# Kernel optimization log

Measured on AMD Instinct MI355X. Metric: run time of the kernel, lower is better.

Reference implementation:

```python
import jax, jax.numpy as jnp
import numpy as np

N_NODES = 10000
N_EDGES = 640000
D_FEAT = 128
D_OUT = 128


def setup_inputs() -> dict:
    key = jax.random.key(0)
    ks = jax.random.split(key, 7)
    feat = jax.random.normal(ks[0], (N_NODES, D_FEAT), dtype=jnp.float32)
    # src_fc: Linear(D_FEAT, D_FEAT); fc: Linear(2*D_FEAT, D_OUT). torch Linear weight is [out, in].
    W_src = jax.random.normal(ks[1], (D_FEAT, D_FEAT), dtype=jnp.float32) * (1.0 / np.sqrt(D_FEAT))
    b_src = jax.random.normal(ks[2], (D_FEAT,), dtype=jnp.float32) * 0.01
    W_fc = jax.random.normal(ks[3], (D_OUT, 2 * D_FEAT), dtype=jnp.float32) * (1.0 / np.sqrt(2 * D_FEAT))
    b_fc = jax.random.normal(ks[4], (D_OUT,), dtype=jnp.float32) * 0.01
    src = jax.random.randint(ks[5], (N_EDGES,), 0, N_NODES, dtype=jnp.int32)
    dst = jax.random.randint(ks[6], (N_EDGES,), 0, N_NODES, dtype=jnp.int32)
    return {"feat": feat, "W_src": W_src, "b_src": b_src, "W_fc": W_fc, "b_fc": b_fc,
            "src": src, "dst": dst}


def reference(feat, W_src, b_src, W_fc, b_fc, src, dst):
    """SAGEConv forward (eval mode: dropout = identity, activation = identity).

    message: m_e = src_fc(feat[src_e])                 # [E, D]
    reduce:  neigh_v = mean_{e: dst_e = v} m_e         # [N, D]
    apply:   h_v = fc(concat(feat_v, neigh_v))         # [N, D_out]
    """
    n = feat.shape[0]
    # gather src features and apply per-edge linear transform
    m = feat[src] @ W_src.T + b_src                                  # [E, D]
    # segment mean over destination nodes (nodes with no in-edges get 0,
    # matching DGL's zero-initialized dstdata)
    agg = jax.ops.segment_sum(m, dst, num_segments=n)                # [N, D]
    deg = jax.ops.segment_sum(jnp.ones(dst.shape, feat.dtype), dst, num_segments=n)
    neigh = agg / jnp.maximum(deg, 1.0)[:, None]                     # [N, D]
    h = jnp.concatenate([feat, neigh], axis=-1) @ W_fc.T + b_fc      # [N, D_out]
    return h
```

## Files before the change

kernel.cpp:

```cpp
#include <hip/hip_runtime.h>

#define NN 10000
#define DF 128
#define NE 640000
#define GBN 16
#define NBUCK 625
#define TILE 8192
#define NTILES ((NE + TILE - 1) / TILE)
#define EPT 8
#define GCAP 2048

#define PACK_BLKS 625
#define PREP_BLKS 16

typedef __attribute__((ext_vector_type(8))) short bf16x8;
typedef __attribute__((ext_vector_type(4))) float f32x4;
typedef unsigned long long ull;

__device__ __forceinline__ unsigned int f2bf(float f) {
    unsigned int u = __float_as_uint(f);
    u = (u + 0x7FFFu + ((u >> 16) & 1u)) >> 16;
    return u;
}
__device__ __forceinline__ unsigned int pack2bf(float a, float b) {
    return f2bf(a) | (f2bf(b) << 16);
}
__device__ __forceinline__ float bf_lo(unsigned int v) { return __uint_as_float(v << 16); }
__device__ __forceinline__ float bf_hi(unsigned int v) { return __uint_as_float(v & 0xFFFF0000u); }

__global__ __launch_bounds__(1024) void prologue(const float* __restrict__ feat,
                                                 unsigned int* __restrict__ A_bf,
                                                 const int* __restrict__ dstv,
                                                 int* __restrict__ tbl,
                                                 const float* __restrict__ Wfc,
                                                 const float* __restrict__ Wsrc,
                                                 const float* __restrict__ bsrc,
                                                 unsigned int* __restrict__ Bw,
                                                 float* __restrict__ bsrc2)
{
    const int bx = blockIdx.x, tid = threadIdx.x;

    if (bx < PACK_BLKS) {
        const int id = bx * 1024 + tid;
        const int row = id >> 6, j = id & 63;
        const float2 f = *(const float2*)(feat + (size_t)row * DF + 2 * j);
        A_bf[(size_t)row * 64 + j] = pack2bf(f.x, f.y);
        return;
    }
    if (bx < PACK_BLKS + NTILES) {
        __shared__ int h[NBUCK];
        const int t = bx - PACK_BLKS;
        if (tid < NBUCK) h[tid] = 0;
        __syncthreads();
        const int e0 = t * TILE;
#pragma unroll
        for (int j = 0; j < EPT; ++j) {
            const int e = e0 + j * 1024 + tid;
            if (e < NE) atomicAdd(&h[dstv[e] >> 4], 1);
        }
        __syncthreads();
        if (tid < NBUCK) tbl[t * NBUCK + tid] = h[tid];
        return;
    }
    {
        __shared__ float wp[8][128];
        __shared__ float red[16];
        const int g = tid >> 7;
        const int k = tid & 127;
        const int o = (bx - PACK_BLKS - NTILES) * 8 + g;
        const float* w2 = Wfc + (size_t)o * 256 + 128;
        float acc = 0.f;
#pragma unroll 8
        for (int j = 0; j < 128; ++j)
            acc = fmaf(w2[j], Wsrc[j * 128 + k], acc);
        wp[g][k] = acc;

        float p = w2[k] * bsrc[k];
#pragma unroll
        for (int d = 32; d > 0; d >>= 1) p += __shfl_down(p, d);
        if ((tid & 63) == 0) red[tid >> 6] = p;
        __syncthreads();
        if (k < 64) {
            const float2 wf = *(const float2*)(Wfc + (size_t)o * 256 + 2 * k);
            Bw[(size_t)o * 128 + k] = pack2bf(wf.x, wf.y);
            Bw[(size_t)o * 128 + 64 + k] = pack2bf(wp[g][2 * k], wp[g][2 * k + 1]);
        }
        if (k == 0) bsrc2[o] = red[2 * g] + red[2 * g + 1];
    }
}

__global__ __launch_bounds__(1024) void bin2(const int* __restrict__ srcv,
                                             const int* __restrict__ dstv,
                                             const int* __restrict__ tbl,
                                             unsigned int* __restrict__ ents,
                                             int* __restrict__ off_g)
{
    __shared__ unsigned int ent[TILE];
    __shared__ ull sc[1024];
    __shared__ int lbase[NBUCK];
    __shared__ int lcur[NBUCK];
    __shared__ int gbase[NBUCK];

    const int tid = threadIdx.x;
    const int bx = blockIdx.x;
    const int e0 = bx * TILE;
    const int n = min(TILE, NE - e0);

    int myd[EPT], mys[EPT];
#pragma unroll
    for (int j = 0; j < EPT; ++j) {
        const int e = e0 + j * 1024 + tid;
        if (e < NE) { myd[j] = dstv[e]; mys[j] = srcv[e]; }
        else { myd[j] = -1; mys[j] = 0; }
    }

    int pre = 0, tot = 0, myh = 0;
    if (tid < NBUCK) {
        for (int t = 0; t < NTILES; ++t) {
            const int c = tbl[t * NBUCK + tid];
            pre += (t < bx) ? c : 0;
            myh += (t == bx) ? c : 0;
            tot += c;
        }
    }
    sc[tid] = (tid < NBUCK) ? (((ull)(unsigned)tot << 32) | (unsigned)myh) : 0ull;
    __syncthreads();
    for (int d = 1; d < 1024; d <<= 1) {
        ull x = (tid >= d) ? sc[tid - d] : 0ull;
        __syncthreads();
        sc[tid] += x;
        __syncthreads();
    }
    const ull ex = (tid == 0) ? 0ull : sc[tid - 1];
    if (tid < NBUCK) {
        const int offb = (int)(ex >> 32);
        lbase[tid] = (int)(ex & 0xFFFFFFFFull);
        gbase[tid] = offb + pre;
        lcur[tid] = 0;
        if (bx == 0) off_g[tid] = offb;
    }
    if (bx == 0 && tid == NBUCK - 1) off_g[NBUCK] = (int)(sc[NBUCK - 1] >> 32);
    __syncthreads();

#pragma unroll
    for (int j = 0; j < EPT; ++j) {
        if (myd[j] >= 0) {
            const int b = myd[j] >> 4;
            const int p = atomicAdd(&lcur[b], 1);
            ent[lbase[b] + p] = ((unsigned)myd[j] << 14) | (unsigned)mys[j];
        }
    }
    __syncthreads();

    for (int i = tid; i < n; i += 1024) {
        const unsigned u = ent[i];
        const int b = (int)(u >> 18);
        ents[gbase[b] + (i - lbase[b])] = u;
    }
}

__global__ __launch_bounds__(256) void gather_apply(const unsigned int* __restrict__ A_bf,
                                                    const unsigned int* __restrict__ Bw,
                                                    const unsigned int* __restrict__ ents,
                                                    const int* __restrict__ off,
                                                    const float* __restrict__ bfc,
                                                    const float* __restrict__ bsrc2,
                                                    float* __restrict__ out)
{
    __shared__ unsigned int raw[GCAP];
    __shared__ unsigned short sorted[GCAP];
    __shared__ int h[GBN], base[GBN], cur[GBN];
    __shared__ unsigned int ntile[GBN][68];

    const int tid = threadIdx.x;
    const int b = blockIdx.x;
    const int rbase = b * GBN;
    const int r0 = off[b], r1 = off[b + 1];
    const int cnt = min(r1 - r0, GCAP);

    if (tid < GBN) { h[tid] = 0; cur[tid] = 0; }
    __syncthreads();
    for (int i = tid; i < cnt; i += 256) {
        const unsigned u = ents[r0 + i];
        raw[i] = u;
        atomicAdd(&h[(u >> 14) & (GBN - 1)], 1);
    }
    __syncthreads();
    if (tid == 0) {
        int s = 0;
#pragma unroll
        for (int j = 0; j < GBN; ++j) { base[j] = s; s += h[j]; }
    }
    __syncthreads();
    for (int i = tid; i < cnt; i += 256) {
        const unsigned u = raw[i];
        const int dl = (int)((u >> 14) & (GBN - 1));
        const int p = base[dl] + atomicAdd(&cur[dl], 1);
        sorted[p] = (unsigned short)(u & 0x3FFFu);
    }
    __syncthreads();

    const int wave = tid >> 6, lane = tid & 63;
#pragma unroll
    for (int j = 0; j < 4; ++j) {
        const int dl = wave * 4 + j;
        const int s0 = base[dl], n = h[dl];
        float ax = 0.f, ay = 0.f;
        int i = 0;
        for (; i + 4 <= n; i += 4) {
            const int ia = sorted[s0 + i + 0];
            const int ib = sorted[s0 + i + 1];
            const int ic = sorted[s0 + i + 2];
            const int id = sorted[s0 + i + 3];
            const unsigned a  = A_bf[(size_t)ia * 64 + lane];
            const unsigned bb = A_bf[(size_t)ib * 64 + lane];
            const unsigned c  = A_bf[(size_t)ic * 64 + lane];
            const unsigned d  = A_bf[(size_t)id * 64 + lane];
            ax += (bf_lo(a) + bf_lo(bb)) + (bf_lo(c) + bf_lo(d));
            ay += (bf_hi(a) + bf_hi(bb)) + (bf_hi(c) + bf_hi(d));
        }
        for (; i < n; ++i) {
            const unsigned a = A_bf[(size_t)sorted[s0 + i] * 64 + lane];
            ax += bf_lo(a); ay += bf_hi(a);
        }
        const float inv = (n > 0) ? 1.f / (float)n : 0.f;
        ntile[dl][lane] = pack2bf(ax * inv, ay * inv);
    }
    __syncthreads();

    const int wv = wave;
    const int r = lane & 15, kg = lane >> 4;

    const unsigned int* ap = A_bf + (size_t)(rbase + r) * 64 + kg * 4;
    bf16x8 a[8];
#pragma unroll
    for (int s = 0; s < 4; ++s) a[s] = *(const bf16x8*)(ap + s * 16);
#pragma unroll
    for (int s = 0; s < 4; ++s) a[4 + s] = *(const bf16x8*)(&ntile[r][s * 16 + kg * 4]);

    bool hd[4];
#pragma unroll
    for (int q = 0; q < 4; ++q) hd[q] = h[kg * 4 + q] > 0;

#pragma unroll
    for (int half = 0; half < 2; ++half) {
        const int cbase = (wv * 2 + half) * 16;
        const unsigned int* bp = Bw + (size_t)(cbase + r) * 128 + kg * 4;
        bf16x8 bb[8];
#pragma unroll
        for (int s = 0; s < 8; ++s) bb[s] = *(const bf16x8*)(bp + s * 16);
        f32x4 acc = {0.f, 0.f, 0.f, 0.f};
#pragma unroll
        for (int s = 0; s < 8; ++s)
            acc = __builtin_amdgcn_mfma_f32_16x16x32_bf16(a[s], bb[s], acc, 0, 0, 0);

        const int col = cbase + r;
        const float bc = bfc[col], bs = bsrc2[col];
#pragma unroll
        for (int q = 0; q < 4; ++q) {
            const int row = rbase + kg * 4 + q;
            out[(size_t)row * DF + col] = acc[q] + bc + (hd[q] ? bs : 0.f);
        }
    }
}

extern "C" void kernel_launch(void* const* d_in, const int* in_sizes, int n_in,
                              void* d_out, int out_size, void* d_ws, size_t ws_size,
                              hipStream_t stream) {
    const float* feat  = (const float*)d_in[0];
    const float* W_src = (const float*)d_in[1];
    const float* b_src = (const float*)d_in[2];
    const float* W_fc  = (const float*)d_in[3];
    const float* b_fc  = (const float*)d_in[4];
    const int*   src   = (const int*)d_in[5];
    const int*   dst   = (const int*)d_in[6];
    float* out = (float*)d_out;

    unsigned int* A_bf = (unsigned int*)d_ws;
    unsigned int* Bw = A_bf + (size_t)NN * 64;
    float* bsrc2 = (float*)(Bw + 128 * 128);
    int*   off   = (int*)(bsrc2 + 128);
    int*   tbl   = off + (NBUCK + 1);
    unsigned int* ents = (unsigned int*)(tbl + (size_t)NTILES * NBUCK);

    prologue    <<<PACK_BLKS + NTILES + PREP_BLKS, 1024, 0, stream>>>(
                    feat, A_bf, dst, tbl, W_fc, W_src, b_src, Bw, bsrc2);
    bin2        <<<NTILES, 1024, 0, stream>>>(src, dst, tbl, ents, off);
    gather_apply<<<NBUCK, 256, 0, stream>>>(A_bf, Bw, ents, off, b_fc, bsrc2, out);
}
```

Before: 56.46 us.

## Vectorize bf16 packing, use wave-shuffle scan, double gather_apply threads

The feature-to-bf16 pack now has each thread convert 8 floats with 128-bit loads and stores, so it needs far fewer blocks. The bucket prefix scan in bin2 replaces the 1024-entry shared-memory Hillis-Steele scan, which needed many barriers, with wave shuffles plus a small per-wave partial sum. gather_apply now runs 512 threads per block: each wave aggregates 2 destination rows with 8 loads in flight instead of 4 rows with 4, and computes one 16-column MFMA tile instead of two. The aim is more parallelism and memory-level parallelism in the latency-bound gather, at the cost of more registers per thread and higher block-size pressure.

```diff
diff --git a/kernel.cpp b/kernel.cpp
--- a/kernel.cpp
+++ b/kernel.cpp
@@ -10,7 +10,7 @@
 #define EPT 8
 #define GCAP 2048
 
-#define PACK_BLKS 625
+#define PACK_BLKS 157
 #define PREP_BLKS 16
 
 typedef __attribute__((ext_vector_type(8))) short bf16x8;
@@ -42,9 +42,15 @@
 
     if (bx < PACK_BLKS) {
         const int id = bx * 1024 + tid;
-        const int row = id >> 6, j = id & 63;
-        const float2 f = *(const float2*)(feat + (size_t)row * DF + 2 * j);
-        A_bf[(size_t)row * 64 + j] = pack2bf(f.x, f.y);
+        if (id < NN * 16) {
+            const int row = id >> 4, j4 = id & 15;
+            const float4 fa = *(const float4*)(feat + (size_t)row * DF + 8 * j4);
+            const float4 fb = *(const float4*)(feat + (size_t)row * DF + 8 * j4 + 4);
+            uint4 v;
+            v.x = pack2bf(fa.x, fa.y); v.y = pack2bf(fa.z, fa.w);
+            v.z = pack2bf(fb.x, fb.y); v.w = pack2bf(fb.z, fb.w);
+            *(uint4*)(A_bf + (size_t)row * 64 + 4 * j4) = v;
+        }
         return;
     }
     if (bx < PACK_BLKS + NTILES) {
@@ -96,12 +102,13 @@
                                              int* __restrict__ off_g)
 {
     __shared__ unsigned int ent[TILE];
-    __shared__ ull sc[1024];
+    __shared__ ull wpart[16];
     __shared__ int lbase[NBUCK];
     __shared__ int lcur[NBUCK];
     __shared__ int gbase[NBUCK];
 
     const int tid = threadIdx.x;
+    const int lane = tid & 63, wid = tid >> 6;
     const int bx = blockIdx.x;
     const int e0 = bx * TILE;
     const int n = min(TILE, NE - e0);
@@ -123,23 +130,28 @@
             tot += c;
         }
     }
-    sc[tid] = (tid < NBUCK) ? (((ull)(unsigned)tot << 32) | (unsigned)myh) : 0ull;
-    __syncthreads();
-    for (int d = 1; d < 1024; d <<= 1) {
-        ull x = (tid >= d) ? sc[tid - d] : 0ull;
-        __syncthreads();
-        sc[tid] += x;
-        __syncthreads();
-    }
-    const ull ex = (tid == 0) ? 0ull : sc[tid - 1];
+    const ull v = (tid < NBUCK) ? (((ull)(unsigned)tot << 32) | (unsigned)myh) : 0ull;
+    ull inc = v;
+#pragma unroll
+    for (int d = 1; d < 64; d <<= 1) {
+        const ull x = (ull)__shfl_up((unsigned long long)inc, d);
+        if (lane >= d) inc += x;
+    }
+    if (lane == 63) wpart[wid] = inc;
+    __syncthreads();
+    ull wsum = 0;
+    for (int w = 0; w < wid; ++w) wsum += wpart[w];
+    const ull ex = wsum + inc - v;
     if (tid < NBUCK) {
         const int offb = (int)(ex >> 32);
         lbase[tid] = (int)(ex & 0xFFFFFFFFull);
         gbase[tid] = offb + pre;
         lcur[tid] = 0;
-        if (bx == 0) off_g[tid] = offb;
-    }
-    if (bx == 0 && tid == NBUCK - 1) off_g[NBUCK] = (int)(sc[NBUCK - 1] >> 32);
+        if (bx == 0) {
+            off_g[tid] = offb;
+            if (tid == NBUCK - 1) off_g[NBUCK] = (int)((ex + v) >> 32);
+        }
+    }
     __syncthreads();
 
 #pragma unroll
@@ -159,7 +171,7 @@
     }
 }
 
-__global__ __launch_bounds__(256) void gather_apply(const unsigned int* __restrict__ A_bf,
+__global__ __launch_bounds__(512) void gather_apply(const unsigned int* __restrict__ A_bf,
                                                     const unsigned int* __restrict__ Bw,
                                                     const unsigned int* __restrict__ ents,
                                                     const int* __restrict__ off,
@@ -180,7 +192,7 @@
 
     if (tid < GBN) { h[tid] = 0; cur[tid] = 0; }
     __syncthreads();
-    for (int i = tid; i < cnt; i += 256) {
+    for (int i = tid; i < cnt; i += 512) {
         const unsigned u = ents[r0 + i];
         raw[i] = u;
         atomicAdd(&h[(u >> 14) & (GBN - 1)], 1);
@@ -192,7 +204,7 @@
         for (int j = 0; j < GBN; ++j) { base[j] = s; s += h[j]; }
     }
     __syncthreads();
-    for (int i = tid; i < cnt; i += 256) {
+    for (int i = tid; i < cnt; i += 512) {
         const unsigned u = raw[i];
         const int dl = (int)((u >> 14) & (GBN - 1));
         const int p = base[dl] + atomicAdd(&cur[dl], 1);
@@ -202,22 +214,18 @@
 
     const int wave = tid >> 6, lane = tid & 63;
 #pragma unroll
-    for (int j = 0; j < 4; ++j) {
-        const int dl = wave * 4 + j;
+    for (int j = 0; j < 2; ++j) {
+        const int dl = wave * 2 + j;
         const int s0 = base[dl], n = h[dl];
         float ax = 0.f, ay = 0.f;
         int i = 0;
-        for (; i + 4 <= n; i += 4) {
-            const int ia = sorted[s0 + i + 0];
-            const int ib = sorted[s0 + i + 1];
-            const int ic = sorted[s0 + i + 2];
-            const int id = sorted[s0 + i + 3];
-            const unsigned a  = A_bf[(size_t)ia * 64 + lane];
-            const unsigned bb = A_bf[(size_t)ib * 64 + lane];
-            const unsigned c  = A_bf[(size_t)ic * 64 + lane];
-            const unsigned d  = A_bf[(size_t)id * 64 + lane];
-            ax += (bf_lo(a) + bf_lo(bb)) + (bf_lo(c) + bf_lo(d));
-            ay += (bf_hi(a) + bf_hi(bb)) + (bf_hi(c) + bf_hi(d));
+        for (; i + 8 <= n; i += 8) {
+            unsigned w[8];
+#pragma unroll
+            for (int q = 0; q < 8; ++q)
+                w[q] = A_bf[(size_t)sorted[s0 + i + q] * 64 + lane];
+#pragma unroll
+            for (int q = 0; q < 8; ++q) { ax += bf_lo(w[q]); ay += bf_hi(w[q]); }
         }
         for (; i < n; ++i) {
             const unsigned a = A_bf[(size_t)sorted[s0 + i] * 64 + lane];
@@ -228,7 +236,6 @@
     }
     __syncthreads();
 
-    const int wv = wave;
     const int r = lane & 15, kg = lane >> 4;
 
     const unsigned int* ap = A_bf + (size_t)(rbase + r) * 64 + kg * 4;
@@ -242,25 +249,22 @@
 #pragma unroll
     for (int q = 0; q < 4; ++q) hd[q] = h[kg * 4 + q] > 0;
 
-#pragma unroll
-    for (int half = 0; half < 2; ++half) {
-        const int cbase = (wv * 2 + half) * 16;
-        const unsigned int* bp = Bw + (size_t)(cbase + r) * 128 + kg * 4;
-        bf16x8 bb[8];
-#pragma unroll
-        for (int s = 0; s < 8; ++s) bb[s] = *(const bf16x8*)(bp + s * 16);
-        f32x4 acc = {0.f, 0.f, 0.f, 0.f};
-#pragma unroll
-        for (int s = 0; s < 8; ++s)
-            acc = __builtin_amdgcn_mfma_f32_16x16x32_bf16(a[s], bb[s], acc, 0, 0, 0);
-
-        const int col = cbase + r;
-        const float bc = bfc[col], bs = bsrc2[col];
-#pragma unroll
-        for (int q = 0; q < 4; ++q) {
-            const int row = rbase + kg * 4 + q;
-            out[(size_t)row * DF + col] = acc[q] + bc + (hd[q] ? bs : 0.f);
-        }
+    const int cbase = wave * 16;
+    const unsigned int* bp = Bw + (size_t)(cbase + r) * 128 + kg * 4;
+    bf16x8 bb[8];
+#pragma unroll
+    for (int s = 0; s < 8; ++s) bb[s] = *(const bf16x8*)(bp + s * 16);
+    f32x4 acc = {0.f, 0.f, 0.f, 0.f};
+#pragma unroll
+    for (int s = 0; s < 8; ++s)
+        acc = __builtin_amdgcn_mfma_f32_16x16x32_bf16(a[s], bb[s], acc, 0, 0, 0);
+
+    const int col = cbase + r;
+    const float bc = bfc[col], bs = bsrc2[col];
+#pragma unroll
+    for (int q = 0; q < 4; ++q) {
+        const int row = rbase + kg * 4 + q;
+        out[(size_t)row * DF + col] = acc[q] + bc + (hd[q] ? bs : 0.f);
     }
 }
 
@@ -286,5 +290,5 @@
     prologue    <<<PACK_BLKS + NTILES + PREP_BLKS, 1024, 0, stream>>>(
                     feat, A_bf, dst, tbl, W_fc, W_src, b_src, Bw, bsrc2);
     bin2        <<<NTILES, 1024, 0, stream>>>(src, dst, tbl, ents, off);
-    gather_apply<<<NBUCK, 256, 0, stream>>>(A_bf, Bw, ents, off, b_fc, bsrc2, out);
-}
+    gather_apply<<<NBUCK, 512, 0, stream>>>(A_bf, Bw, ents, off, b_fc, bsrc2, out);
+}
```

Result: faster. 53.18 us (-5.8%).
